# Kernel tuning notes

Measured on AMD Instinct MI355X. Metric: run time of the kernel, lower is better.

Reference implementation:

```python
import jax, jax.numpy as jnp
import numpy as np

A_CONST = 0.1
B_CONST = 0.2
C_CONST = 0.8

INPUT_SIZE = 1024
HIDDEN_SIZE = 2048
BATCH = 32768
SIGMA = 0.02


def acti_func(x, a, b, c):
    # piecewise: a*(1 - x/b) for x<=b ; 0 for b<x<c ; a*(x-c)/(1-c) for x>=c
    low = -a * x / b + a
    high = a * x / (1.0 - c) + a * c / (c - 1.0)
    return jnp.where(x <= b, low, jnp.where(x >= c, high, jnp.zeros_like(x)))


def setup_inputs() -> dict:
    key = jax.random.key(0)
    ks = jax.random.split(key, 4)
    x = jax.random.normal(ks[0], (BATCH, INPUT_SIZE), dtype=jnp.float32)
    W0 = jax.random.normal(ks[1], (INPUT_SIZE, HIDDEN_SIZE), dtype=jnp.float32) * SIGMA
    b0 = jnp.zeros((HIDDEN_SIZE,), dtype=jnp.float32)
    W1 = jax.random.normal(ks[2], (HIDDEN_SIZE, HIDDEN_SIZE), dtype=jnp.float32) * SIGMA
    b1 = jnp.zeros((HIDDEN_SIZE,), dtype=jnp.float32)
    W2 = jax.random.normal(ks[3], (HIDDEN_SIZE, 1), dtype=jnp.float32) * SIGMA
    b2 = jnp.zeros((1,), dtype=jnp.float32)
    return {"x": x, "W0": W0, "b0": b0, "W1": W1, "b1": b1, "W2": W2, "b2": b2}


def reference(x, W0, b0, W1, b1, W2, b2):
    h = jax.nn.elu(x @ W0 + b0)
    h = jax.nn.elu(h @ W1 + b1)
    out = jax.nn.sigmoid(h @ W2 + b2)  # [B, 1]
    alpha = acti_func(out, A_CONST, B_CONST, C_CONST)
    return out, alpha
```

## Files before the change

### kernel.cpp

```cpp
#include <hip/hip_runtime.h>
#include <hip/hip_bf16.h>
#include <stdint.h>

typedef unsigned short u16;
typedef __bf16 bf16x8 __attribute__((ext_vector_type(8)));
typedef float floatx4 __attribute__((ext_vector_type(4)));

__device__ __forceinline__ u16 f2bf(float f) {
  union { float f; unsigned u; } c; c.f = f;
  unsigned r = c.u + 0x7fffu + ((c.u >> 16) & 1u);
  return (u16)(r >> 16);
}

__device__ __forceinline__ void load_lds16(const void* g, void* l) {
  __builtin_amdgcn_global_load_lds(
      (const __attribute__((address_space(1))) void*)g,
      (__attribute__((address_space(3))) void*)l,
      16, 0, 0);
}

__device__ __forceinline__ void memclob() { asm volatile("" ::: "memory"); }
__device__ __forceinline__ void barrier_() {
  memclob();
  __builtin_amdgcn_s_barrier();
  memclob();
}

__global__ __launch_bounds__(256) void preamble(
    const float* __restrict__ x, const float* __restrict__ W0,
    const float* __restrict__ W1,
    u16* __restrict__ Xb, u16* __restrict__ Wt0, u16* __restrict__ Wt1,
    float* __restrict__ z)
{
  __shared__ float tile[32][33];
  const int bid = blockIdx.x;
  const int t = threadIdx.x;

  if (bid < 32768) {
    int i = bid * 256 + t;
    float4 f = ((const float4*)x)[i];
    ushort4 u;
    u.x = f2bf(f.x); u.y = f2bf(f.y); u.z = f2bf(f.z); u.w = f2bf(f.w);
    ((ushort4*)Xb)[i] = u;
  } else if (bid < 32768 + 2048) {
    int tb = bid - 32768;
    int bx = (tb & 63) * 32, by = (tb >> 6) * 32;
    int tx = t & 31, ty = t >> 5;
    #pragma unroll
    for (int i = 0; i < 32; i += 8)
      tile[ty + i][tx] = W0[(size_t)(by + ty + i) * 2048 + bx + tx];
    __syncthreads();
    #pragma unroll
    for (int i = 0; i < 32; i += 8)
      Wt0[(size_t)(bx + ty + i) * 1024 + by + tx] = f2bf(tile[tx][ty + i]);
  } else if (bid < 32768 + 2048 + 4096) {
    int tb = bid - (32768 + 2048);
    int bx = (tb & 63) * 32, by = (tb >> 6) * 32;
    int tx = t & 31, ty = t >> 5;
    #pragma unroll
    for (int i = 0; i < 32; i += 8)
      tile[ty + i][tx] = W1[(size_t)(by + ty + i) * 2048 + bx + tx];
    __syncthreads();
    #pragma unroll
    for (int i = 0; i < 32; i += 8)
      Wt1[(size_t)(bx + ty + i) * 2048 + by + tx] = f2bf(tile[tx][ty + i]);
  } else {
    int tb = bid - (32768 + 2048 + 4096);
    ((float4*)z)[tb * 256 + t] = (float4){0.f, 0.f, 0.f, 0.f};
  }
}

template<bool FUSE_HEAD, int KK>
__global__ __launch_bounds__(512, 2) void gemm256_q4(
    const u16* __restrict__ A,
    const u16* __restrict__ Bt,
    const float* __restrict__ bias,
    u16* __restrict__ C,
    const float* __restrict__ W2,
    float* __restrict__ z,
    int M, int N)
{
  __shared__ u16 lds[65536];

  const int t = threadIdx.x;
  const int l = t & 63;
  const int w = t >> 6;
  const int wm = w >> 2;
  const int wn = w & 3;
  const int lm = l & 15;
  const int q  = l >> 4;

  const int nwg = gridDim.x;
  int wg = blockIdx.x;
  wg = (wg & 7) * (nwg >> 3) + (wg >> 3);
  const int nbn = N >> 8;
  const int n0 = (wg % nbn) << 8;
  const int m0 = (wg / nbn) << 8;

  const int rowoff = t >> 3;
  const int lc8 = ((t & 7) ^ (rowoff & 7)) * 8;
  const int bq = rowoff >> 5;
  const int br = rowoff & 31;
  const u16* rA0 = A  + (size_t)(m0 + rowoff) * KK + lc8;
  const u16* rA1 = A  + (size_t)(m0 + 128 + rowoff) * KK + lc8;
  const u16* rB0 = Bt + (size_t)(n0 + bq * 64 + br) * KK + lc8;
  const u16* rB1 = Bt + (size_t)(n0 + (2 + bq) * 64 + br) * KK + lc8;
  const int ldst = t * 8;

#define SLOT(p, idx) (((p) * 4 + (idx)) * 8192)

#define STG_A(P, S, KOFF) do {                                                 \
    load_lds16(rA0 + (S) * 64 * KK + (KOFF), &lds[SLOT(P, S) + ldst]);         \
    load_lds16(rA1 + (S) * 64 * KK + (KOFF), &lds[SLOT(P, S) + 4096 + ldst]);  \
  } while (0)
#define STG_B(P, S, KOFF) do {                                                 \
    load_lds16(rB0 + (S) * 32 * KK + (KOFF), &lds[SLOT(P, 2 + (S)) + ldst]);   \
    load_lds16(rB1 + (S) * 32 * KK + (KOFF), &lds[SLOT(P, 2 + (S)) + 4096 + ldst]); \
  } while (0)

  const int ck0 = ((0 * 4 + q) ^ (lm & 7)) * 8;
  const int ck1 = ((1 * 4 + q) ^ (lm & 7)) * 8;
  const int arow = (wm * 64 + lm) * 64;
  const int brow = (wn * 32 + lm) * 64;
#define RDA(p, i, ck) (*(const bf16x8*)&lds[SLOT(p, (i) >> 2) + arow + ((i) & 3) * 1024 + (ck)])
#define RDB(p, j, ck) (*(const bf16x8*)&lds[SLOT(p, 2 + ((j) >> 1)) + brow + ((j) & 1) * 1024 + (ck)])
#define MFMA(d, x, y) d = __builtin_amdgcn_mfma_f32_16x16x32_bf16(x, y, d, 0, 0, 0)

  floatx4 acc[8][4];
  #pragma unroll
  for (int i = 0; i < 8; ++i)
    #pragma unroll
    for (int j = 0; j < 4; ++j)
      acc[i][j] = (floatx4){0.f, 0.f, 0.f, 0.f};

  bf16x8 a0[4][2];
  bf16x8 a1[4][2];
  bf16x8 bl[2][2];
  bf16x8 bh[2][2];

  constexpr int NK = KK >> 6;
  static_assert(NK >= 4 && (NK & 1) == 0, "NK must be even, >= 4");

#define VMW6 asm volatile("s_waitcnt vmcnt(6)" ::: "memory")
#define VMW0 asm volatile("s_waitcnt vmcnt(0)" ::: "memory")
#define VMWN do {} while (0)

#define KTILE(P, SAH, KO1, S2, KO2, VMW)                                       \
  {                                                                            \
        \
    _Pragma("unroll")                                                          \
    for (int i = 0; i < 4; ++i) { a0[i][0] = RDA(P, i, ck0); a0[i][1] = RDA(P, i, ck1); } \
    _Pragma("unroll")                                                          \
    for (int j = 0; j < 2; ++j) { bl[j][0] = RDB(P, j, ck0); bl[j][1] = RDB(P, j, ck1); } \
    if (SAH) { STG_A((P) ^ 1, 1, KO1); }                                       \
    barrier_();                                                                \
    __builtin_amdgcn_s_setprio(1);                                             \
    _Pragma("unroll")                                                          \
    for (int i = 0; i < 4; ++i)                                                \
      _Pragma("unroll")                                                        \
      for (int j = 0; j < 2; ++j) {                                            \
        MFMA(acc[i][j], a0[i][0], bl[j][0]);                                   \
        MFMA(acc[i][j], a0[i][1], bl[j][1]);                                   \
      }                                                                        \
    __builtin_amdgcn_s_setprio(0);                                             \
                                \
    _Pragma("unroll")                                                          \
    for (int j = 0; j < 2; ++j) { bh[j][0] = RDB(P, 2 + j, ck0); bh[j][1] = RDB(P, 2 + j, ck1); } \
    barrier_();                                                                \
    __builtin_amdgcn_s_setprio(1);                                             \
    _Pragma("unroll")                                                          \
    for (int i = 0; i < 4; ++i)                                                \
      _Pragma("unroll")                                                        \
      for (int j = 0; j < 2; ++j) {                                            \
        MFMA(acc[i][2 + j], a0[i][0], bh[j][0]);                               \
        MFMA(acc[i][2 + j], a0[i][1], bh[j][1]);                               \
      }                                                                        \
    __builtin_amdgcn_s_setprio(0);                                             \
         \
    _Pragma("unroll")                                                          \
    for (int i = 0; i < 4; ++i) { a1[i][0] = RDA(P, 4 + i, ck0); a1[i][1] = RDA(P, 4 + i, ck1); } \
    if (S2) { STG_A(P, 0, KO2); STG_B(P, 0, KO2); }                            \
    barrier_();                                                                \
    __builtin_amdgcn_s_setprio(1);                                             \
    _Pragma("unroll")                                                          \
    for (int i = 0; i < 4; ++i)                                                \
      _Pragma("unroll")                                                        \
      for (int j = 0; j < 2; ++j) {                                            \
        MFMA(acc[4 + i][j], a1[i][0], bl[j][0]);                               \
        MFMA(acc[4 + i][j], a1[i][1], bl[j][1]);                               \
      }                                                                        \
    __builtin_amdgcn_s_setprio(0);                                             \
    \
    if (S2) { STG_B(P, 1, KO2); }                                              \
    VMW;                                                                       \
    barrier_();                                                                \
    __builtin_amdgcn_s_setprio(1);                                             \
    _Pragma("unroll")                                                          \
    for (int i = 0; i < 4; ++i)                                                \
      _Pragma("unroll")                                                        \
      for (int j = 0; j < 2; ++j) {                                            \
        MFMA(acc[4 + i][2 + j], a1[i][0], bh[j][0]);                           \
        MFMA(acc[4 + i][2 + j], a1[i][1], bh[j][1]);                           \
      }                                                                        \
    __builtin_amdgcn_s_setprio(0);                                             \
  }

  STG_A(0, 0, 0); memclob(); STG_A(0, 1, 0); memclob();
  STG_B(0, 0, 0); memclob(); STG_B(0, 1, 0); memclob();
  STG_A(1, 0, 64); memclob(); STG_B(1, 0, 64); memclob(); STG_B(1, 1, 64);
  VMW6;
  barrier_();

  #pragma unroll 1
  for (int g = 0; g < NK - 2; g += 2) {
    KTILE(0, true, 64, true, 128, VMW6);
    KTILE(1, true, 128, true, 192, VMW6);
    rA0 += 128; rA1 += 128; rB0 += 128; rB1 += 128;
  }
  KTILE(0, true, 64, false, 0, VMW0);
  KTILE(1, false, 0, false, 0, VMWN);

  float bv[4];
  #pragma unroll
  for (int j = 0; j < 4; ++j) bv[j] = bias[n0 + wn * 64 + j * 16 + lm];

  if (!FUSE_HEAD) {
    #pragma unroll
    for (int i = 0; i < 8; ++i) {
      #pragma unroll
      for (int r = 0; r < 4; ++r) {
        int grow = m0 + wm * 128 + i * 16 + q * 4 + r;
        size_t base = (size_t)grow * N + n0 + wn * 64 + lm;
        #pragma unroll
        for (int j = 0; j < 4; ++j) {
          float v = acc[i][j][r] + bv[j];
          v = v > 0.f ? v : (__expf(v) - 1.f);
          C[base + j * 16] = f2bf(v);
        }
      }
    }
  } else {
    float w2v[4];
    #pragma unroll
    for (int j = 0; j < 4; ++j) w2v[j] = W2[n0 + wn * 64 + j * 16 + lm];
    #pragma unroll
    for (int i = 0; i < 8; ++i) {
      #pragma unroll
      for (int r = 0; r < 4; ++r) {
        float pacc = 0.f;
        #pragma unroll
        for (int j = 0; j < 4; ++j) {
          float v = acc[i][j][r] + bv[j];
          v = v > 0.f ? v : (__expf(v) - 1.f);
          pacc += v * w2v[j];
        }
        pacc += __shfl_xor(pacc, 1);
        pacc += __shfl_xor(pacc, 2);
        pacc += __shfl_xor(pacc, 4);
        pacc += __shfl_xor(pacc, 8);
        if (lm == 0) atomicAdd(&z[m0 + wm * 128 + i * 16 + q * 4 + r], pacc);
      }
    }
  }
#undef SLOT
#undef STG_A
#undef STG_B
#undef RDA
#undef RDB
#undef MFMA
#undef KTILE
#undef VMW6
#undef VMW0
#undef VMWN
}

__global__ __launch_bounds__(256) void sigmoid_alpha(
    const float* __restrict__ z, const float* __restrict__ b2,
    float* __restrict__ out, int B)
{
  int i = blockIdx.x * blockDim.x + threadIdx.x;
  if (i >= B) return;
  float o = 1.f / (1.f + expf(-(z[i] + b2[0])));
  float alpha;
  if (o <= 0.2f)      alpha = 0.1f - 0.5f * o;
  else if (o >= 0.8f) alpha = 0.5f * o - 0.4f;
  else                alpha = 0.f;
  out[i] = o;
  out[B + i] = alpha;
}

extern "C" void kernel_launch(void* const* d_in, const int* in_sizes, int n_in,
                              void* d_out, int out_size, void* d_ws, size_t ws_size,
                              hipStream_t stream) {
  const int BATCH = 32768, HID = 2048;

  const float* x  = (const float*)d_in[0];
  const float* W0 = (const float*)d_in[1];
  const float* b0 = (const float*)d_in[2];
  const float* W1 = (const float*)d_in[3];
  const float* b1 = (const float*)d_in[4];
  const float* W2 = (const float*)d_in[5];
  const float* b2 = (const float*)d_in[6];
  float* out = (float*)d_out;

  char* ws = (char*)d_ws;
  u16* Xb   = (u16*)(ws);
  u16* Wt0  = (u16*)(ws + (size_t)67108864);
  u16* Wt1  = (u16*)(ws + (size_t)71303168);
  u16* h0   = (u16*)(ws + (size_t)79691776);
  float* z  = (float*)(ws + (size_t)213909504);

  const int grid = (BATCH / 256) * (HID / 256);

  preamble<<<32768 + 2048 + 4096 + 32, 256, 0, stream>>>(x, W0, W1, Xb, Wt0, Wt1, z);
  gemm256_q4<false, 1024><<<grid, 512, 0, stream>>>(
      Xb, Wt0, b0, h0, nullptr, nullptr, BATCH, HID);
  gemm256_q4<true, 2048><<<grid, 512, 0, stream>>>(
      h0, Wt1, b1, nullptr, W2, z, BATCH, HID);
  sigmoid_alpha<<<BATCH / 256, 256, 0, stream>>>(z, b2, out, BATCH);
}
```

Before: 573.6 us.

## Software-pipeline LDS fragment reads across k-tiles with sched barriers

Restructures the GEMM k-tile loop so the A/B register fragments for the next k-tile are read from LDS during the last MFMA phases of the current tile, instead of at the start of each tile before the first barrier. It adds sched_barrier fences to pin the placement of LDS reads, global-to-LDS staging and MFMAs, removes the s_setprio toggling, and merges the two row-pointer pairs into single base pointers with a constant offset. This is meant to hide LDS read latency behind matrix math. In exchange it raises register pressure and moves the staging of the A half-tile into new slots, which risks LDS read/write ordering hazards.

New measurement: 757.3 us. +32.0%, slower.

```diff
diff --git a/kernel.cpp b/kernel.cpp
--- a/kernel.cpp
+++ b/kernel.cpp
@@ -25,6 +25,8 @@
   __builtin_amdgcn_s_barrier();
   memclob();
 }
+#define SCHB __builtin_amdgcn_sched_barrier(0)
+#define BARS do { barrier_(); SCHB; } while (0)
 
 __global__ __launch_bounds__(256) void preamble(
     const float* __restrict__ x, const float* __restrict__ W0,
@@ -71,7 +73,7 @@
 }
 
 template<bool FUSE_HEAD, int KK>
-__global__ __launch_bounds__(512, 2) void gemm256_q4(
+__global__ __launch_bounds__(512, 2) void gemm256_pl(
     const u16* __restrict__ A,
     const u16* __restrict__ Bt,
     const float* __restrict__ bias,
@@ -101,21 +103,19 @@
   const int lc8 = ((t & 7) ^ (rowoff & 7)) * 8;
   const int bq = rowoff >> 5;
   const int br = rowoff & 31;
-  const u16* rA0 = A  + (size_t)(m0 + rowoff) * KK + lc8;
-  const u16* rA1 = A  + (size_t)(m0 + 128 + rowoff) * KK + lc8;
-  const u16* rB0 = Bt + (size_t)(n0 + bq * 64 + br) * KK + lc8;
-  const u16* rB1 = Bt + (size_t)(n0 + (2 + bq) * 64 + br) * KK + lc8;
+  const u16* rA = A  + (size_t)(m0 + rowoff) * KK + lc8;
+  const u16* rB = Bt + (size_t)(n0 + bq * 64 + br) * KK + lc8;
   const int ldst = t * 8;
 
 #define SLOT(p, idx) (((p) * 4 + (idx)) * 8192)
 
 #define STG_A(P, S, KOFF) do {                                                 \
-    load_lds16(rA0 + (S) * 64 * KK + (KOFF), &lds[SLOT(P, S) + ldst]);         \
-    load_lds16(rA1 + (S) * 64 * KK + (KOFF), &lds[SLOT(P, S) + 4096 + ldst]);  \
+    load_lds16(rA + (S) * 64 * KK + (KOFF), &lds[SLOT(P, S) + ldst]);          \
+    load_lds16(rA + (S) * 64 * KK + 128 * KK + (KOFF), &lds[SLOT(P, S) + 4096 + ldst]); \
   } while (0)
 #define STG_B(P, S, KOFF) do {                                                 \
-    load_lds16(rB0 + (S) * 32 * KK + (KOFF), &lds[SLOT(P, 2 + (S)) + ldst]);   \
-    load_lds16(rB1 + (S) * 32 * KK + (KOFF), &lds[SLOT(P, 2 + (S)) + 4096 + ldst]); \
+    load_lds16(rB + (S) * 32 * KK + (KOFF), &lds[SLOT(P, 2 + (S)) + ldst]);    \
+    load_lds16(rB + (S) * 32 * KK + 128 * KK + (KOFF), &lds[SLOT(P, 2 + (S)) + 4096 + ldst]); \
   } while (0)
 
   const int ck0 = ((0 * 4 + q) ^ (lm & 7)) * 8;
@@ -145,16 +145,9 @@
 #define VMW0 asm volatile("s_waitcnt vmcnt(0)" ::: "memory")
 #define VMWN do {} while (0)
 
-#define KTILE(P, SAH, KO1, S2, KO2, VMW)                                       \
+#define KTILE(P, RDNEXT, S2, KO, VMW)                                          \
   {                                                                            \
-        \
-    _Pragma("unroll")                                                          \
-    for (int i = 0; i < 4; ++i) { a0[i][0] = RDA(P, i, ck0); a0[i][1] = RDA(P, i, ck1); } \
-    _Pragma("unroll")                                                          \
-    for (int j = 0; j < 2; ++j) { bl[j][0] = RDB(P, j, ck0); bl[j][1] = RDB(P, j, ck1); } \
-    if (SAH) { STG_A((P) ^ 1, 1, KO1); }                                       \
-    barrier_();                                                                \
-    __builtin_amdgcn_s_setprio(1);                                             \
+    BARS;                                                            \
     _Pragma("unroll")                                                          \
     for (int i = 0; i < 4; ++i)                                                \
       _Pragma("unroll")                                                        \
@@ -162,12 +155,9 @@
         MFMA(acc[i][j], a0[i][0], bl[j][0]);                                   \
         MFMA(acc[i][j], a0[i][1], bl[j][1]);                                   \
       }                                                                        \
-    __builtin_amdgcn_s_setprio(0);                                             \
-                                \
-    _Pragma("unroll")                                                          \
-    for (int j = 0; j < 2; ++j) { bh[j][0] = RDB(P, 2 + j, ck0); bh[j][1] = RDB(P, 2 + j, ck1); } \
-    barrier_();                                                                \
-    __builtin_amdgcn_s_setprio(1);                                             \
+    _Pragma("unroll")                                                          \
+    for (int i = 0; i < 4; ++i) { a1[i][0] = RDA(P, 4 + i, ck0); a1[i][1] = RDA(P, 4 + i, ck1); } \
+    BARS;                                                            \
     _Pragma("unroll")                                                          \
     for (int i = 0; i < 4; ++i)                                                \
       _Pragma("unroll")                                                        \
@@ -175,13 +165,8 @@
         MFMA(acc[i][2 + j], a0[i][0], bh[j][0]);                               \
         MFMA(acc[i][2 + j], a0[i][1], bh[j][1]);                               \
       }                                                                        \
-    __builtin_amdgcn_s_setprio(0);                                             \
-         \
-    _Pragma("unroll")                                                          \
-    for (int i = 0; i < 4; ++i) { a1[i][0] = RDA(P, 4 + i, ck0); a1[i][1] = RDA(P, 4 + i, ck1); } \
-    if (S2) { STG_A(P, 0, KO2); STG_B(P, 0, KO2); }                            \
-    barrier_();                                                                \
-    __builtin_amdgcn_s_setprio(1);                                             \
+    if (S2) { STG_A(P, 0, KO); STG_B(P, 0, KO); }                              \
+    BARS;                                                            \
     _Pragma("unroll")                                                          \
     for (int i = 0; i < 4; ++i)                                                \
       _Pragma("unroll")                                                        \
@@ -189,12 +174,17 @@
         MFMA(acc[4 + i][j], a1[i][0], bl[j][0]);                               \
         MFMA(acc[4 + i][j], a1[i][1], bl[j][1]);                               \
       }                                                                        \
-    __builtin_amdgcn_s_setprio(0);                                             \
-    \
-    if (S2) { STG_B(P, 1, KO2); }                                              \
+    SCHB;                          \
+    if (S2) { STG_B(P, 1, KO); }                                               \
     VMW;                                                                       \
-    barrier_();                                                                \
-    __builtin_amdgcn_s_setprio(1);                                             \
+    BARS;                                                    \
+    if (RDNEXT) {                                                              \
+      _Pragma("unroll")                                                        \
+      for (int i = 0; i < 4; ++i) { a0[i][0] = RDA((P) ^ 1, i, ck0); a0[i][1] = RDA((P) ^ 1, i, ck1); } \
+      _Pragma("unroll")                                                        \
+      for (int j = 0; j < 2; ++j) { bl[j][0] = RDB((P) ^ 1, j, ck0); bl[j][1] = RDB((P) ^ 1, j, ck1); } \
+    }                                                                          \
+    SCHB; \
     _Pragma("unroll")                                                          \
     for (int i = 0; i < 4; ++i)                                                \
       _Pragma("unroll")                                                        \
@@ -202,23 +192,36 @@
         MFMA(acc[4 + i][2 + j], a1[i][0], bh[j][0]);                           \
         MFMA(acc[4 + i][2 + j], a1[i][1], bh[j][1]);                           \
       }                                                                        \
-    __builtin_amdgcn_s_setprio(0);                                             \
+    SCHB;             \
+    if (RDNEXT) {                                                              \
+      _Pragma("unroll")                                                        \
+      for (int j = 0; j < 2; ++j) { bh[j][0] = RDB((P) ^ 1, 2 + j, ck0); bh[j][1] = RDB((P) ^ 1, 2 + j, ck1); } \
+    }                                                                          \
+    if (S2) { STG_A(P, 1, KO); } \
   }
 
   STG_A(0, 0, 0); memclob(); STG_A(0, 1, 0); memclob();
   STG_B(0, 0, 0); memclob(); STG_B(0, 1, 0); memclob();
   STG_A(1, 0, 64); memclob(); STG_B(1, 0, 64); memclob(); STG_B(1, 1, 64);
   VMW6;
-  barrier_();
+  BARS;
+  #pragma unroll
+  for (int i = 0; i < 4; ++i) { a0[i][0] = RDA(0, i, ck0); a0[i][1] = RDA(0, i, ck1); }
+  #pragma unroll
+  for (int j = 0; j < 2; ++j) { bl[j][0] = RDB(0, j, ck0); bl[j][1] = RDB(0, j, ck1); }
+  SCHB;
+  #pragma unroll
+  for (int j = 0; j < 2; ++j) { bh[j][0] = RDB(0, 2 + j, ck0); bh[j][1] = RDB(0, 2 + j, ck1); }
+  STG_A(1, 1, 64);
 
   #pragma unroll 1
   for (int g = 0; g < NK - 2; g += 2) {
-    KTILE(0, true, 64, true, 128, VMW6);
-    KTILE(1, true, 128, true, 192, VMW6);
-    rA0 += 128; rA1 += 128; rB0 += 128; rB1 += 128;
+    KTILE(0, true, true, 128, VMW6);
+    KTILE(1, true, true, 192, VMW6);
+    rA += 128; rB += 128;
   }
-  KTILE(0, true, 64, false, 0, VMW0);
-  KTILE(1, false, 0, false, 0, VMWN);
+  KTILE(0, true, false, 0, VMW0);
+  KTILE(1, false, false, 0, VMWN);
 
   float bv[4];
   #pragma unroll
@@ -313,9 +316,9 @@
   const int grid = (BATCH / 256) * (HID / 256);
 
   preamble<<<32768 + 2048 + 4096 + 32, 256, 0, stream>>>(x, W0, W1, Xb, Wt0, Wt1, z);
-  gemm256_q4<false, 1024><<<grid, 512, 0, stream>>>(
+  gemm256_pl<false, 1024><<<grid, 512, 0, stream>>>(
       Xb, Wt0, b0, h0, nullptr, nullptr, BATCH, HID);
-  gemm256_q4<true, 2048><<<grid, 512, 0, stream>>>(
+  gemm256_pl<true, 2048><<<grid, 512, 0, stream>>>(
       h0, Wt1, b1, nullptr, W2, z, BATCH, HID);
   sigmoid_alpha<<<BATCH / 256, 256, 0, stream>>>(z, b2, out, BATCH);
 }
```
